# Kernel optimization log

Measured on AMD Instinct MI355X. Metric: run time of the kernel, lower is better.

Reference implementation:

```python
import jax, jax.numpy as jnp
import numpy as np

N_NODES = 100000
N_EDGES = 1600000
IN_CH = 128
DIM = 128
OUT_CH = 10
NUM_GRAPHS = 128
BN_EPS = 1e-5


def _bn_train(h, gamma, beta):
    # BatchNorm1d in training mode: batch statistics over the node axis
    mean = jnp.mean(h, axis=0)
    var = jnp.var(h, axis=0)
    return (h - mean) * jax.lax.rsqrt(var + BN_EPS) * gamma + beta


def _gin_conv(x, src, dst, W1, b1, gamma, beta, W2, b2):
    # GINConv with eps=0: nn(x + sum_{j in N(i)} x_j)
    agg = jax.ops.segment_sum(x[src], dst, num_segments=x.shape[0])  # [N, d]
    h = (x + agg) @ W1 + b1
    h = jax.nn.relu(_bn_train(h, gamma, beta))
    h = jax.nn.relu(h @ W2 + b2)
    return h


def setup_inputs() -> dict:
    key = jax.random.key(0)
    ks = jax.random.split(key, 16)
    s = 0.02
    inp = {
        "x": jax.random.normal(ks[0], (N_NODES, IN_CH), dtype=jnp.float32),
        "edge_index": jax.random.randint(ks[1], (2, N_EDGES), 0, N_NODES, dtype=jnp.int64),
        "batch": jnp.sort(jax.random.randint(ks[2], (N_NODES,), 0, NUM_GRAPHS, dtype=jnp.int64)),
        # conv1 MLP
        "W1a": jax.random.normal(ks[3], (IN_CH, DIM), dtype=jnp.float32) * s,
        "b1a": jnp.zeros((DIM,), jnp.float32),
        "ga": jnp.ones((DIM,), jnp.float32),
        "ba": jnp.zeros((DIM,), jnp.float32),
        "W2a": jax.random.normal(ks[4], (DIM, DIM), dtype=jnp.float32) * s,
        "b2a": jnp.zeros((DIM,), jnp.float32),
        # conv2 MLP
        "W1b": jax.random.normal(ks[5], (DIM, DIM), dtype=jnp.float32) * s,
        "b1b": jnp.zeros((DIM,), jnp.float32),
        "gb": jnp.ones((DIM,), jnp.float32),
        "bb": jnp.zeros((DIM,), jnp.float32),
        "W2b": jax.random.normal(ks[6], (DIM, DIM), dtype=jnp.float32) * s,
        "b2b": jnp.zeros((DIM,), jnp.float32),
        # readout linears
        "Wl1": jax.random.normal(ks[7], (DIM, DIM), dtype=jnp.float32) * s,
        "bl1": jnp.zeros((DIM,), jnp.float32),
        "Wl2": jax.random.normal(ks[8], (DIM, OUT_CH), dtype=jnp.float32) * s,
        "bl2": jnp.zeros((OUT_CH,), jnp.float32),
    }
    return inp


def reference(x, edge_index, batch, W1a, b1a, ga, ba, W2a, b2a,
              W1b, b1b, gb, bb, W2b, b2b, Wl1, bl1, Wl2, bl2):
    src, dst = edge_index[0], edge_index[1]
    h = _gin_conv(x, src, dst, W1a, b1a, ga, ba, W2a, b2a)
    h = _gin_conv(h, src, dst, W1b, b1b, gb, bb, W2b, b2b)
    pooled = jax.ops.segment_sum(h, batch, num_segments=NUM_GRAPHS)  # [G, d]
    out = jax.nn.relu(pooled @ Wl1 + bl1)
    # dropout p=0.5 is identity in deterministic/eval evaluation
    out = out @ Wl2 + bl2
    return out
```

## Files before the change

### kernel.cpp

```cpp
#include <hip/hip_runtime.h>

#define N_NODES    100000
#define N_EDGES    1600000
#define DIM        128
#define OUT_CH     10
#define NUM_GRAPHS 128
#define BN_EPS     1e-5f

#define BSHIFT   8
#define NB2      391
#define CAP2     5120

typedef __attribute__((ext_vector_type(8))) short short8;
typedef __attribute__((ext_vector_type(4))) float floatx4;

__device__ inline float bf2f(unsigned short u) {
    union { unsigned i; float f; } v; v.i = (unsigned)u << 16; return v.f;
}
__device__ inline unsigned short f2bf(float f) {
    union { float f; unsigned i; } v; v.f = f;
    unsigned r = (v.i + 0x7fffu + ((v.i >> 16) & 1u)) >> 16;
    return (unsigned short)r;
}

__device__ inline void async_cp16(const unsigned short* g, unsigned short* l) {
    __builtin_amdgcn_global_load_lds(
        (const __attribute__((address_space(1))) void*)g,
        (__attribute__((address_space(3))) void*)l, 16, 0, 0);
}

__global__ __launch_bounds__(256)
void k_bucket(const int* __restrict__ src, const int* __restrict__ dst,
              int* __restrict__ gcur, uint2* __restrict__ pairs) {
    __shared__ int h[NB2];
    int t = threadIdx.x;
    for (int i = t; i < NB2; i += 256) h[i] = 0;
    __syncthreads();
    int base = blockIdx.x * 4096;
    #pragma unroll
    for (int i = 0; i < 16; ++i) {
        int idx = base + i * 256 + t;
        if (idx < N_EDGES) atomicAdd(&h[dst[idx] >> BSHIFT], 1);
    }
    __syncthreads();
    for (int i = t; i < NB2; i += 256) h[i] = atomicAdd(&gcur[i], h[i]);
    __syncthreads();
    #pragma unroll
    for (int i = 0; i < 16; ++i) {
        int idx = base + i * 256 + t;
        if (idx < N_EDGES) {
            int d = dst[idx];
            int b = d >> BSHIFT;
            int pos = atomicAdd(&h[b], 1);
            if (pos < CAP2) pairs[(size_t)b * CAP2 + pos] = make_uint2((unsigned)src[idx], (unsigned)d);
        }
    }
}

__global__ void k_bscan(const int* __restrict__ gcur, int* __restrict__ bbase,
                        int* __restrict__ row_ptr) {
    __shared__ int sh[512];
    int t = threadIdx.x;
    int v = (t < NB2) ? min(gcur[t], CAP2) : 0;
    sh[t] = v; __syncthreads();
    for (int off = 1; off < 512; off <<= 1) {
        int tmp = (t >= off) ? sh[t - off] : 0;
        __syncthreads();
        sh[t] += tmp;
        __syncthreads();
    }
    if (t < NB2) bbase[t] = sh[t] - v;
    if (t == NB2 - 1) { bbase[NB2] = sh[t]; row_ptr[N_NODES] = sh[t]; }
}

__global__ __launch_bounds__(256)
void k_csr(const uint2* __restrict__ pairs, const int* __restrict__ gcur,
           const int* __restrict__ bbase, int* __restrict__ row_ptr,
           int* __restrict__ col) {
    __shared__ int hist[256];
    __shared__ int cur[256];
    int bi = blockIdx.x, t = threadIdx.x;
    hist[t] = 0; __syncthreads();
    int n = min(gcur[bi], CAP2);
    const uint2* P = pairs + (size_t)bi * CAP2;
    for (int i = t; i < n; i += 256)
        atomicAdd(&hist[P[i].y & 255], 1);
    __syncthreads();
    int self = hist[t];
    cur[t] = self; __syncthreads();
    for (int off = 1; off < 256; off <<= 1) {
        int tmp = (t >= off) ? cur[t - off] : 0;
        __syncthreads();
        cur[t] += tmp;
        __syncthreads();
    }
    int excl = cur[t] - self;
    int base = bbase[bi];
    int node = (bi << 8) + t;
    if (node < N_NODES) row_ptr[node] = base + excl;
    __syncthreads();
    cur[t] = base + excl;
    __syncthreads();
    for (int i = t; i < n; i += 256) {
        uint2 e = P[i];
        int pos = atomicAdd(&cur[e.y & 255], 1);
        col[pos] = (int)e.x;
    }
}

__global__ void k_cvt_x(const float* __restrict__ x, unsigned short* __restrict__ xb) {
    int idx = blockIdx.x * 256 + threadIdx.x;
    float4 v = ((const float4*)x)[idx];
    ushort4 o;
    o.x = f2bf(v.x); o.y = f2bf(v.y); o.z = f2bf(v.z); o.w = f2bf(v.w);
    ((ushort4*)xb)[idx] = o;
}

__global__ void k_prep_w(const float* __restrict__ W0, const float* __restrict__ W1,
                         const float* __restrict__ W2, const float* __restrict__ W3,
                         unsigned short* __restrict__ Wt) {
    const float* Ws[4] = {W0, W1, W2, W3};
    const float* W = Ws[blockIdx.y];
    unsigned short* o = Wt + blockIdx.y * (DIM * DIM);
    int idx = blockIdx.x * 256 + threadIdx.x;
    int n = idx >> 7, k = idx & 127;
    o[idx] = f2bf(W[k * DIM + n]);
}

__global__ void k_agg(const unsigned short* __restrict__ X,
                      unsigned short* __restrict__ Out,
                      const int* __restrict__ row_ptr, const int* __restrict__ col) {
    int wid = (blockIdx.x * 256 + threadIdx.x) >> 6;
    if (wid >= N_NODES) return;
    int lane = threadIdx.x & 63;
    int half = lane >> 5, m = lane & 31;
    const ushort4* X4 = (const ushort4*)X;

    float a0=0.f,a1=0.f,a2=0.f,a3=0.f;
    float c0=0.f,c1=0.f,c2=0.f,c3=0.f;
    if (half == 0) {
        ushort4 sv = X4[(size_t)wid * 32 + m];
        a0 = bf2f(sv.x); a1 = bf2f(sv.y); a2 = bf2f(sv.z); a3 = bf2f(sv.w);
    }
    int s = row_ptr[wid], e = row_ptr[wid + 1];
    int p = s + half;
    for (; p + 6 < e; p += 8) {
        int n0 = col[p], n1 = col[p + 2], n2 = col[p + 4], n3 = col[p + 6];
        ushort4 v0 = X4[(size_t)n0 * 32 + m];
        ushort4 v1 = X4[(size_t)n1 * 32 + m];
        ushort4 v2 = X4[(size_t)n2 * 32 + m];
        ushort4 v3 = X4[(size_t)n3 * 32 + m];
        a0 += bf2f(v0.x); a1 += bf2f(v0.y); a2 += bf2f(v0.z); a3 += bf2f(v0.w);
        c0 += bf2f(v1.x); c1 += bf2f(v1.y); c2 += bf2f(v1.z); c3 += bf2f(v1.w);
        a0 += bf2f(v2.x); a1 += bf2f(v2.y); a2 += bf2f(v2.z); a3 += bf2f(v2.w);
        c0 += bf2f(v3.x); c1 += bf2f(v3.y); c2 += bf2f(v3.z); c3 += bf2f(v3.w);
    }
    for (; p < e; p += 2) {
        ushort4 v = X4[(size_t)col[p] * 32 + m];
        a0 += bf2f(v.x); a1 += bf2f(v.y); a2 += bf2f(v.z); a3 += bf2f(v.w);
    }
    a0 += c0; a1 += c1; a2 += c2; a3 += c3;
    a0 += __shfl_xor(a0, 32);
    a1 += __shfl_xor(a1, 32);
    a2 += __shfl_xor(a2, 32);
    a3 += __shfl_xor(a3, 32);
    if (half == 0) {
        ushort4 o;
        o.x = f2bf(a0); o.y = f2bf(a1); o.z = f2bf(a2); o.w = f2bf(a3);
        ((ushort4*)Out)[(size_t)wid * 32 + m] = o;
    }
}

template<bool BN_LOAD, bool RELU_ST>
__global__ __launch_bounds__(256)
void k_gemm(const unsigned short* __restrict__ In, unsigned short* __restrict__ Out,
            const unsigned short* __restrict__ Wt, const float* __restrict__ bias,
            const float* __restrict__ scale, const float* __restrict__ shift) {
    __shared__ __align__(16) unsigned short sB[128 * 128];
    __shared__ float ssc[128], ssh[128];

    int t = threadIdx.x;
    int w = t >> 6, lane = t & 63;
    int r0 = blockIdx.x * 128;
    int m = lane & 15;
    int q = lane >> 4;

    int rowA0 = min(r0 + w * 32 + m,      N_NODES - 1);
    int rowA1 = min(r0 + w * 32 + 16 + m, N_NODES - 1);
    short8 a0[4], a1[4];
    #pragma unroll
    for (int kk = 0; kk < 4; ++kk) {
        a0[kk] = *(const short8*)(In + (size_t)rowA0 * 128 + kk * 32 + q * 8);
        a1[kk] = *(const short8*)(In + (size_t)rowA1 * 128 + kk * 32 + q * 8);
    }

    #pragma unroll
    for (int u = 0; u < 8; ++u) {
        int i = (w * 8 + u) * 64 + lane;
        int n = i >> 4, p = i & 15;
        async_cp16(Wt + n * 128 + ((p ^ (n & 7)) << 3), sB + (size_t)(w * 8 + u) * 512);
    }
    if (BN_LOAD && t < 128) { ssc[t] = scale[t]; ssh[t] = shift[t]; }
    __syncthreads();

    if (BN_LOAD) {
        #pragma unroll
        for (int kk = 0; kk < 4; ++kk) {
            int base = kk * 32 + q * 8;
            float4 c0 = *(const float4*)&ssc[base];
            float4 c1 = *(const float4*)&ssc[base + 4];
            float4 h0 = *(const float4*)&ssh[base];
            float4 h1 = *(const float4*)&ssh[base + 4];
            float sc[8] = {c0.x,c0.y,c0.z,c0.w,c1.x,c1.y,c1.z,c1.w};
            float sh[8] = {h0.x,h0.y,h0.z,h0.w,h1.x,h1.y,h1.z,h1.w};
            #pragma unroll
            for (int j = 0; j < 8; ++j) {
                float f0 = fmaxf(bf2f((unsigned short)a0[kk][j]) * sc[j] + sh[j], 0.f);
                float f1 = fmaxf(bf2f((unsigned short)a1[kk][j]) * sc[j] + sh[j], 0.f);
                a0[kk][j] = (short)f2bf(f0);
                a1[kk][j] = (short)f2bf(f1);
            }
        }
    }

    int sw = m & 7;
    floatx4 acc[2][8] = {};
    #pragma unroll
    for (int kk = 0; kk < 4; ++kk) {
        int cp = (kk * 4 + q) ^ sw;
        #pragma unroll
        for (int c = 0; c < 8; ++c) {
            int nr = c * 16 + m;
            short8 b = *(const short8*)&sB[nr * 128 + (cp << 3)];
            acc[0][c] = __builtin_amdgcn_mfma_f32_16x16x32_bf16(b, a0[kk], acc[0][c], 0, 0, 0);
            acc[1][c] = __builtin_amdgcn_mfma_f32_16x16x32_bf16(b, a1[kk], acc[1][c], 0, 0, 0);
        }
    }

    #pragma unroll
    for (int c = 0; c < 8; ++c) {
        int ch0 = c * 16 + q * 4;
        float4 bv = *(const float4*)(bias + ch0);
        #pragma unroll
        for (int h = 0; h < 2; ++h) {
            int node = r0 + w * 32 + h * 16 + m;
            if (node < N_NODES) {
                float v0 = acc[h][c][0] + bv.x;
                float v1 = acc[h][c][1] + bv.y;
                float v2 = acc[h][c][2] + bv.z;
                float v3 = acc[h][c][3] + bv.w;
                if (RELU_ST) {
                    v0 = fmaxf(v0, 0.f); v1 = fmaxf(v1, 0.f);
                    v2 = fmaxf(v2, 0.f); v3 = fmaxf(v3, 0.f);
                }
                ushort4 o;
                o.x = f2bf(v0); o.y = f2bf(v1); o.z = f2bf(v2); o.w = f2bf(v3);
                *(ushort4*)(Out + (size_t)node * 128 + ch0) = o;
            }
        }
    }
}

#define ST_BLOCKS 250
#define ST_ROWS   400
__global__ __launch_bounds__(256)
void k_stats(const unsigned short* __restrict__ H,
             float* __restrict__ ssum, float* __restrict__ ssq) {
    __shared__ float rs[8][128];
    __shared__ float rq[8][128];
    int t  = threadIdx.x;
    int cq = t & 31;
    int r  = t >> 5;
    int row0 = blockIdx.x * ST_ROWS;
    float s0=0,s1=0,s2=0,s3=0,q0=0,q1=0,q2=0,q3=0;
    for (int i = r; i < ST_ROWS; i += 8) {
        ushort4 v = *(const ushort4*)(H + (size_t)(row0 + i) * 128 + cq * 4);
        float f0=bf2f(v.x), f1=bf2f(v.y), f2=bf2f(v.z), f3=bf2f(v.w);
        s0+=f0; s1+=f1; s2+=f2; s3+=f3;
        q0+=f0*f0; q1+=f1*f1; q2+=f2*f2; q3+=f3*f3;
    }
    rs[r][cq*4+0]=s0; rs[r][cq*4+1]=s1; rs[r][cq*4+2]=s2; rs[r][cq*4+3]=s3;
    rq[r][cq*4+0]=q0; rq[r][cq*4+1]=q1; rq[r][cq*4+2]=q2; rq[r][cq*4+3]=q3;
    __syncthreads();
    if (t < 128) {
        float a = 0.f, b = 0.f;
        #pragma unroll
        for (int j = 0; j < 8; ++j) { a += rs[j][t]; b += rq[j][t]; }
        atomicAdd(&ssum[t], a);
        atomicAdd(&ssq [t], b);
    }
}

__global__ void k_bnfin(const float* __restrict__ sum, const float* __restrict__ sq,
                        const float* __restrict__ gamma, const float* __restrict__ beta,
                        float* __restrict__ scale, float* __restrict__ shift) {
    int c = threadIdx.x;
    if (c < DIM) {
        float m   = sum[c] * (1.0f / N_NODES);
        float var = sq[c] * (1.0f / N_NODES) - m * m;
        float inv = rsqrtf(var + BN_EPS);
        float sc  = gamma[c] * inv;
        scale[c] = sc;
        shift[c] = beta[c] - m * sc;
    }
}

#define POOL_BLOCKS 512
#define POOL_CHUNK  196
__global__ void k_pool(const unsigned short* __restrict__ h, const int* __restrict__ batch,
                       float* __restrict__ pooled) {
    int c  = threadIdx.x;
    int n0 = blockIdx.x * POOL_CHUNK;
    if (n0 >= N_NODES) return;
    int n1 = min(n0 + POOL_CHUNK, N_NODES);
    int g = batch[n0];
    float acc = 0.f;
    for (int i = n0; i < n1; ++i) {
        int gi = batch[i];
        if (gi != g) { atomicAdd(&pooled[g * DIM + c], acc); acc = 0.f; g = gi; }
        acc += bf2f(h[(size_t)i * DIM + c]);
    }
    atomicAdd(&pooled[g * DIM + c], acc);
}

__global__ void k_readout1(const float* __restrict__ pooled, const float* __restrict__ W,
                           const float* __restrict__ b, float* __restrict__ r1) {
    int idx = blockIdx.x * 256 + threadIdx.x;
    int g = idx >> 7, c = idx & 127;
    float s = b[c];
    const float* p = pooled + g * DIM;
    #pragma unroll 8
    for (int k = 0; k < DIM; ++k) s += p[k] * W[k * DIM + c];
    r1[idx] = fmaxf(s, 0.f);
}

__global__ void k_readout2(const float* __restrict__ r1, const float* __restrict__ W,
                           const float* __restrict__ b, float* __restrict__ out) {
    int idx = blockIdx.x * 256 + threadIdx.x;
    if (idx >= NUM_GRAPHS * OUT_CH) return;
    int g = idx / OUT_CH, c = idx % OUT_CH;
    float s = b[c];
    const float* r = r1 + g * DIM;
    #pragma unroll 8
    for (int k = 0; k < DIM; ++k) s += r[k] * W[k * OUT_CH + c];
    out[idx] = s;
}

extern "C" void kernel_launch(void* const* d_in, const int* in_sizes, int n_in,
                              void* d_out, int out_size, void* d_ws, size_t ws_size,
                              hipStream_t stream) {
    const float* x   = (const float*)d_in[0];
    const int*   ei  = (const int*)d_in[1];
    const int*   bat = (const int*)d_in[2];
    const float* W1a = (const float*)d_in[3];
    const float* b1a = (const float*)d_in[4];
    const float* ga  = (const float*)d_in[5];
    const float* ba  = (const float*)d_in[6];
    const float* W2a = (const float*)d_in[7];
    const float* b2a = (const float*)d_in[8];
    const float* W1b = (const float*)d_in[9];
    const float* b1b = (const float*)d_in[10];
    const float* gb  = (const float*)d_in[11];
    const float* bbt = (const float*)d_in[12];
    const float* W2b = (const float*)d_in[13];
    const float* b2b = (const float*)d_in[14];
    const float* Wl1 = (const float*)d_in[15];
    const float* bl1 = (const float*)d_in[16];
    const float* Wl2 = (const float*)d_in[17];
    const float* bl2 = (const float*)d_in[18];
    float* out = (float*)d_out;

    const int* src = ei;
    const int* dst = ei + N_EDGES;

    char* w = (char*)d_ws;
    size_t off = 0;
    auto alloc = [&](size_t bytes) -> char* {
        char* p = w + off; off += (bytes + 255) & ~(size_t)255; return p;
    };
    unsigned short* xb   = (unsigned short*)alloc((size_t)N_NODES * DIM * 2);
    unsigned short* nb0  = (unsigned short*)alloc((size_t)N_NODES * DIM * 2);
    unsigned short* nb1  = (unsigned short*)alloc((size_t)N_NODES * DIM * 2);
    unsigned short* Wtb  = (unsigned short*)alloc((size_t)4 * DIM * DIM * 2);
    uint2* pairs   = (uint2*)alloc((size_t)NB2 * CAP2 * 8);
    int*   row_ptr = (int*)  alloc((size_t)(N_NODES + 1) * 4);
    int*   col     = (int*)  alloc((size_t)N_EDGES * 4);
    int*   gcur    = (int*)  alloc((NB2 + 1) * 4);
    int*   bbase   = (int*)  alloc((NB2 + 1) * 4);
    float* ssumA   = (float*)alloc(DIM * 4);
    float* ssqA    = (float*)alloc(DIM * 4);
    float* ssumB   = (float*)alloc(DIM * 4);
    float* ssqB    = (float*)alloc(DIM * 4);
    float* scale   = (float*)alloc(DIM * 4);
    float* shift   = (float*)alloc(DIM * 4);
    float* pooled  = (float*)alloc((size_t)NUM_GRAPHS * DIM * 4);
    float* r1      = (float*)alloc((size_t)NUM_GRAPHS * DIM * 4);

    hipMemsetAsync(gcur,  0, (NB2 + 1) * 4, stream);
    hipMemsetAsync(ssumA, 0, DIM * 4 * 4, stream);
    hipMemsetAsync(pooled,0, (size_t)NUM_GRAPHS * DIM * 4, stream);

    k_bucket<<<(N_EDGES + 4095) / 4096, 256, 0, stream>>>(src, dst, gcur, pairs);
    k_bscan<<<1, 512, 0, stream>>>(gcur, bbase, row_ptr);
    k_csr<<<NB2, 256, 0, stream>>>(pairs, gcur, bbase, row_ptr, col);

    k_cvt_x<<<(N_NODES * DIM / 4) / 256, 256, 0, stream>>>(x, xb);
    k_prep_w<<<dim3(64, 4), 256, 0, stream>>>(W1a, W2a, W1b, W2b, Wtb);
    const unsigned short* Wt1a = Wtb;
    const unsigned short* Wt2a = Wtb + DIM * DIM;
    const unsigned short* Wt1b = Wtb + 2 * DIM * DIM;
    const unsigned short* Wt2b = Wtb + 3 * DIM * DIM;

    int agg_blocks  = (N_NODES * 64) / 256;
    int gemm_blocks = (N_NODES + 127) / 128;

    k_agg<<<agg_blocks, 256, 0, stream>>>(xb, nb0, row_ptr, col);
    k_gemm<false, false><<<gemm_blocks, 256, 0, stream>>>(nb0, nb1, Wt1a, b1a, nullptr, nullptr);
    k_stats<<<ST_BLOCKS, 256, 0, stream>>>(nb1, ssumA, ssqA);
    k_bnfin<<<1, 128, 0, stream>>>(ssumA, ssqA, ga, ba, scale, shift);
    k_gemm<true, true><<<gemm_blocks, 256, 0, stream>>>(nb1, nb0, Wt2a, b2a, scale, shift);
    k_agg<<<agg_blocks, 256, 0, stream>>>(nb0, nb1, row_ptr, col);
    k_gemm<false, false><<<gemm_blocks, 256, 0, stream>>>(nb1, nb0, Wt1b, b1b, nullptr, nullptr);
    k_stats<<<ST_BLOCKS, 256, 0, stream>>>(nb0, ssumB, ssqB);
    k_bnfin<<<1, 128, 0, stream>>>(ssumB, ssqB, gb, bbt, scale, shift);
    k_gemm<true, true><<<gemm_blocks, 256, 0, stream>>>(nb0, nb1, Wt2b, b2b, scale, shift);
    k_pool<<<POOL_BLOCKS, 128, 0, stream>>>(nb1, bat, pooled);
    k_readout1<<<(NUM_GRAPHS * DIM) / 256, 256, 0, stream>>>(pooled, Wl1, bl1, r1);
    k_readout2<<<(NUM_GRAPHS * OUT_CH + 255) / 256, 256, 0, stream>>>(r1, Wl2, bl2, out);
}
```

Measured before the change: 513.0 us.

## Fuse BN stats into GEMM epilogue, pack edge pairs, merge memsets and readouts

The BatchNorm sum and sum-of-squares are now accumulated in the first GEMM's epilogue through wave shuffles, LDS atomics and global atomics. The separate stats and finalize kernels are removed, and the scale and shift are computed inside the second GEMM. Edge bucket pairs are packed into 32 bits (src<<8 | low dst bits), which halves the pairs traffic. The memsets are folded into the convert kernel, and the two readout kernels are merged into one. Together these cut launches and one full read pass over the hidden activations. In exchange, stats now come from fp32 values before bf16 rounding, and more global float atomics run.

Result: no change. 514.2 us (+0.2%).

```diff
diff --git a/kernel.cpp b/kernel.cpp
--- a/kernel.cpp
+++ b/kernel.cpp
@@ -29,9 +29,36 @@
         (__attribute__((address_space(3))) void*)l, 16, 0, 0);
 }
 
+__global__ void k_cvt_x(const float* __restrict__ x, unsigned short* __restrict__ xb,
+                        int* __restrict__ gcur, float* __restrict__ stats4,
+                        float* __restrict__ pooled) {
+    int t = threadIdx.x;
+    if (blockIdx.x == 0) {
+        for (int i = t; i < NB2 + 1; i += 256) gcur[i] = 0;
+        for (int i = t; i < 4 * DIM; i += 256) stats4[i] = 0.f;
+        for (int i = t; i < NUM_GRAPHS * DIM; i += 256) pooled[i] = 0.f;
+    }
+    int idx = blockIdx.x * 256 + t;
+    float4 v = ((const float4*)x)[idx];
+    ushort4 o;
+    o.x = f2bf(v.x); o.y = f2bf(v.y); o.z = f2bf(v.z); o.w = f2bf(v.w);
+    ((ushort4*)xb)[idx] = o;
+}
+
+__global__ void k_prep_w(const float* __restrict__ W0, const float* __restrict__ W1,
+                         const float* __restrict__ W2, const float* __restrict__ W3,
+                         unsigned short* __restrict__ Wt) {
+    const float* Ws[4] = {W0, W1, W2, W3};
+    const float* W = Ws[blockIdx.y];
+    unsigned short* o = Wt + blockIdx.y * (DIM * DIM);
+    int idx = blockIdx.x * 256 + threadIdx.x;
+    int n = idx >> 7, k = idx & 127;
+    o[idx] = f2bf(W[k * DIM + n]);
+}
+
 __global__ __launch_bounds__(256)
 void k_bucket(const int* __restrict__ src, const int* __restrict__ dst,
-              int* __restrict__ gcur, uint2* __restrict__ pairs) {
+              int* __restrict__ gcur, unsigned* __restrict__ pairs) {
     __shared__ int h[NB2];
     int t = threadIdx.x;
     for (int i = t; i < NB2; i += 256) h[i] = 0;
@@ -52,7 +79,8 @@
             int d = dst[idx];
             int b = d >> BSHIFT;
             int pos = atomicAdd(&h[b], 1);
-            if (pos < CAP2) pairs[(size_t)b * CAP2 + pos] = make_uint2((unsigned)src[idx], (unsigned)d);
+            if (pos < CAP2)
+                pairs[(size_t)b * CAP2 + pos] = ((unsigned)src[idx] << 8) | (unsigned)(d & 255);
         }
     }
 }
@@ -74,7 +102,7 @@
 }
 
 __global__ __launch_bounds__(256)
-void k_csr(const uint2* __restrict__ pairs, const int* __restrict__ gcur,
+void k_csr(const unsigned* __restrict__ pairs, const int* __restrict__ gcur,
            const int* __restrict__ bbase, int* __restrict__ row_ptr,
            int* __restrict__ col) {
     __shared__ int hist[256];
@@ -82,9 +110,9 @@
     int bi = blockIdx.x, t = threadIdx.x;
     hist[t] = 0; __syncthreads();
     int n = min(gcur[bi], CAP2);
-    const uint2* P = pairs + (size_t)bi * CAP2;
+    const unsigned* P = pairs + (size_t)bi * CAP2;
     for (int i = t; i < n; i += 256)
-        atomicAdd(&hist[P[i].y & 255], 1);
+        atomicAdd(&hist[P[i] & 255u], 1);
     __syncthreads();
     int self = hist[t];
     cur[t] = self; __syncthreads();
@@ -102,29 +130,10 @@
     cur[t] = base + excl;
     __syncthreads();
     for (int i = t; i < n; i += 256) {
-        uint2 e = P[i];
-        int pos = atomicAdd(&cur[e.y & 255], 1);
-        col[pos] = (int)e.x;
-    }
-}
-
-__global__ void k_cvt_x(const float* __restrict__ x, unsigned short* __restrict__ xb) {
-    int idx = blockIdx.x * 256 + threadIdx.x;
-    float4 v = ((const float4*)x)[idx];
-    ushort4 o;
-    o.x = f2bf(v.x); o.y = f2bf(v.y); o.z = f2bf(v.z); o.w = f2bf(v.w);
-    ((ushort4*)xb)[idx] = o;
-}
-
-__global__ void k_prep_w(const float* __restrict__ W0, const float* __restrict__ W1,
-                         const float* __restrict__ W2, const float* __restrict__ W3,
-                         unsigned short* __restrict__ Wt) {
-    const float* Ws[4] = {W0, W1, W2, W3};
-    const float* W = Ws[blockIdx.y];
-    unsigned short* o = Wt + blockIdx.y * (DIM * DIM);
-    int idx = blockIdx.x * 256 + threadIdx.x;
-    int n = idx >> 7, k = idx & 127;
-    o[idx] = f2bf(W[k * DIM + n]);
+        unsigned e = P[i];
+        int pos = atomicAdd(&cur[e & 255u], 1);
+        col[pos] = (int)(e >> 8);
+    }
 }
 
 __global__ void k_agg(const unsigned short* __restrict__ X,
@@ -171,13 +180,16 @@
     }
 }
 
-template<bool BN_LOAD, bool RELU_ST>
+template<bool BN_LOAD, bool STATS, bool RELU_ST>
 __global__ __launch_bounds__(256)
 void k_gemm(const unsigned short* __restrict__ In, unsigned short* __restrict__ Out,
             const unsigned short* __restrict__ Wt, const float* __restrict__ bias,
-            const float* __restrict__ scale, const float* __restrict__ shift) {
+            const float* __restrict__ ssum_in, const float* __restrict__ ssq_in,
+            const float* __restrict__ gamma, const float* __restrict__ beta,
+            float* __restrict__ ssum_out, float* __restrict__ ssq_out) {
     __shared__ __align__(16) unsigned short sB[128 * 128];
     __shared__ float ssc[128], ssh[128];
+    __shared__ float s_sum[128], s_sq[128];
 
     int t = threadIdx.x;
     int w = t >> 6, lane = t & 63;
@@ -200,23 +212,25 @@
         int n = i >> 4, p = i & 15;
         async_cp16(Wt + n * 128 + ((p ^ (n & 7)) << 3), sB + (size_t)(w * 8 + u) * 512);
     }
-    if (BN_LOAD && t < 128) { ssc[t] = scale[t]; ssh[t] = shift[t]; }
+    if (BN_LOAD && t < 128) {
+        float mn  = ssum_in[t] * (1.0f / N_NODES);
+        float var = ssq_in[t] * (1.0f / N_NODES) - mn * mn;
+        float inv = rsqrtf(var + BN_EPS);
+        float sc  = gamma[t] * inv;
+        ssc[t] = sc; ssh[t] = beta[t] - mn * sc;
+    }
+    if (STATS && t < 128) { s_sum[t] = 0.f; s_sq[t] = 0.f; }
     __syncthreads();
 
     if (BN_LOAD) {
         #pragma unroll
         for (int kk = 0; kk < 4; ++kk) {
             int base = kk * 32 + q * 8;
-            float4 c0 = *(const float4*)&ssc[base];
-            float4 c1 = *(const float4*)&ssc[base + 4];
-            float4 h0 = *(const float4*)&ssh[base];
-            float4 h1 = *(const float4*)&ssh[base + 4];
-            float sc[8] = {c0.x,c0.y,c0.z,c0.w,c1.x,c1.y,c1.z,c1.w};
-            float sh[8] = {h0.x,h0.y,h0.z,h0.w,h1.x,h1.y,h1.z,h1.w};
             #pragma unroll
             for (int j = 0; j < 8; ++j) {
-                float f0 = fmaxf(bf2f((unsigned short)a0[kk][j]) * sc[j] + sh[j], 0.f);
-                float f1 = fmaxf(bf2f((unsigned short)a1[kk][j]) * sc[j] + sh[j], 0.f);
+                float scj = ssc[base + j], shj = ssh[base + j];
+                float f0 = fmaxf(bf2f((unsigned short)a0[kk][j]) * scj + shj, 0.f);
+                float f1 = fmaxf(bf2f((unsigned short)a1[kk][j]) * scj + shj, 0.f);
                 a0[kk][j] = (short)f2bf(f0);
                 a1[kk][j] = (short)f2bf(f1);
             }
@@ -241,67 +255,52 @@
     for (int c = 0; c < 8; ++c) {
         int ch0 = c * 16 + q * 4;
         float4 bv = *(const float4*)(bias + ch0);
+        float sr[4] = {0,0,0,0}, qr[4] = {0,0,0,0};
         #pragma unroll
         for (int h = 0; h < 2; ++h) {
             int node = r0 + w * 32 + h * 16 + m;
+            float v0 = acc[h][c][0] + bv.x;
+            float v1 = acc[h][c][1] + bv.y;
+            float v2 = acc[h][c][2] + bv.z;
+            float v3 = acc[h][c][3] + bv.w;
+            if (RELU_ST) {
+                v0 = fmaxf(v0, 0.f); v1 = fmaxf(v1, 0.f);
+                v2 = fmaxf(v2, 0.f); v3 = fmaxf(v3, 0.f);
+            }
             if (node < N_NODES) {
-                float v0 = acc[h][c][0] + bv.x;
-                float v1 = acc[h][c][1] + bv.y;
-                float v2 = acc[h][c][2] + bv.z;
-                float v3 = acc[h][c][3] + bv.w;
-                if (RELU_ST) {
-                    v0 = fmaxf(v0, 0.f); v1 = fmaxf(v1, 0.f);
-                    v2 = fmaxf(v2, 0.f); v3 = fmaxf(v3, 0.f);
-                }
                 ushort4 o;
                 o.x = f2bf(v0); o.y = f2bf(v1); o.z = f2bf(v2); o.w = f2bf(v3);
                 *(ushort4*)(Out + (size_t)node * 128 + ch0) = o;
+                if (STATS) {
+                    sr[0] += v0; sr[1] += v1; sr[2] += v2; sr[3] += v3;
+                    qr[0] += v0*v0; qr[1] += v1*v1; qr[2] += v2*v2; qr[3] += v3*v3;
+                }
             }
         }
-    }
-}
-
-#define ST_BLOCKS 250
-#define ST_ROWS   400
-__global__ __launch_bounds__(256)
-void k_stats(const unsigned short* __restrict__ H,
-             float* __restrict__ ssum, float* __restrict__ ssq) {
-    __shared__ float rs[8][128];
-    __shared__ float rq[8][128];
-    int t  = threadIdx.x;
-    int cq = t & 31;
-    int r  = t >> 5;
-    int row0 = blockIdx.x * ST_ROWS;
-    float s0=0,s1=0,s2=0,s3=0,q0=0,q1=0,q2=0,q3=0;
-    for (int i = r; i < ST_ROWS; i += 8) {
-        ushort4 v = *(const ushort4*)(H + (size_t)(row0 + i) * 128 + cq * 4);
-        float f0=bf2f(v.x), f1=bf2f(v.y), f2=bf2f(v.z), f3=bf2f(v.w);
-        s0+=f0; s1+=f1; s2+=f2; s3+=f3;
-        q0+=f0*f0; q1+=f1*f1; q2+=f2*f2; q3+=f3*f3;
-    }
-    rs[r][cq*4+0]=s0; rs[r][cq*4+1]=s1; rs[r][cq*4+2]=s2; rs[r][cq*4+3]=s3;
-    rq[r][cq*4+0]=q0; rq[r][cq*4+1]=q1; rq[r][cq*4+2]=q2; rq[r][cq*4+3]=q3;
-    __syncthreads();
-    if (t < 128) {
-        float a = 0.f, b = 0.f;
-        #pragma unroll
-        for (int j = 0; j < 8; ++j) { a += rs[j][t]; b += rq[j][t]; }
-        atomicAdd(&ssum[t], a);
-        atomicAdd(&ssq [t], b);
-    }
-}
-
-__global__ void k_bnfin(const float* __restrict__ sum, const float* __restrict__ sq,
-                        const float* __restrict__ gamma, const float* __restrict__ beta,
-                        float* __restrict__ scale, float* __restrict__ shift) {
-    int c = threadIdx.x;
-    if (c < DIM) {
-        float m   = sum[c] * (1.0f / N_NODES);
-        float var = sq[c] * (1.0f / N_NODES) - m * m;
-        float inv = rsqrtf(var + BN_EPS);
-        float sc  = gamma[c] * inv;
-        scale[c] = sc;
-        shift[c] = beta[c] - m * sc;
+        if (STATS) {
+            #pragma unroll
+            for (int msk = 1; msk <= 8; msk <<= 1) {
+                #pragma unroll
+                for (int r = 0; r < 4; ++r) {
+                    sr[r] += __shfl_xor(sr[r], msk);
+                    qr[r] += __shfl_xor(qr[r], msk);
+                }
+            }
+            if (m == 0) {
+                #pragma unroll
+                for (int r = 0; r < 4; ++r) {
+                    atomicAdd(&s_sum[ch0 + r], sr[r]);
+                    atomicAdd(&s_sq [ch0 + r], qr[r]);
+                }
+            }
+        }
+    }
+    if (STATS) {
+        __syncthreads();
+        if (t < 128) {
+            atomicAdd(&ssum_out[t], s_sum[t]);
+            atomicAdd(&ssq_out [t], s_sq[t]);
+        }
     }
 }
 
@@ -323,27 +322,25 @@
     atomicAdd(&pooled[g * DIM + c], acc);
 }
 
-__global__ void k_readout1(const float* __restrict__ pooled, const float* __restrict__ W,
-                           const float* __restrict__ b, float* __restrict__ r1) {
-    int idx = blockIdx.x * 256 + threadIdx.x;
-    int g = idx >> 7, c = idx & 127;
-    float s = b[c];
-    const float* p = pooled + g * DIM;
+__global__ void k_readout(const float* __restrict__ pooled,
+                          const float* __restrict__ Wl1, const float* __restrict__ bl1,
+                          const float* __restrict__ Wl2, const float* __restrict__ bl2,
+                          float* __restrict__ out) {
+    __shared__ float p[128], r[128];
+    int g = blockIdx.x, c = threadIdx.x;
+    p[c] = pooled[g * DIM + c];
+    __syncthreads();
+    float s = bl1[c];
     #pragma unroll 8
-    for (int k = 0; k < DIM; ++k) s += p[k] * W[k * DIM + c];
-    r1[idx] = fmaxf(s, 0.f);
-}
-
-__global__ void k_readout2(const float* __restrict__ r1, const float* __restrict__ W,
-                           const float* __restrict__ b, float* __restrict__ out) {
-    int idx = blockIdx.x * 256 + threadIdx.x;
-    if (idx >= NUM_GRAPHS * OUT_CH) return;
-    int g = idx / OUT_CH, c = idx % OUT_CH;
-    float s = b[c];
-    const float* r = r1 + g * DIM;
-    #pragma unroll 8
-    for (int k = 0; k < DIM; ++k) s += r[k] * W[k * OUT_CH + c];
-    out[idx] = s;
+    for (int k = 0; k < DIM; ++k) s += p[k] * Wl1[k * DIM + c];
+    r[c] = fmaxf(s, 0.f);
+    __syncthreads();
+    if (c < OUT_CH) {
+        float s2 = bl2[c];
+        #pragma unroll 8
+        for (int k = 0; k < DIM; ++k) s2 += r[k] * Wl2[k * OUT_CH + c];
+        out[g * OUT_CH + c] = s2;
+    }
 }
 
 extern "C" void kernel_launch(void* const* d_in, const int* in_sizes, int n_in,
@@ -382,49 +379,39 @@
     unsigned short* nb0  = (unsigned short*)alloc((size_t)N_NODES * DIM * 2);
     unsigned short* nb1  = (unsigned short*)alloc((size_t)N_NODES * DIM * 2);
     unsigned short* Wtb  = (unsigned short*)alloc((size_t)4 * DIM * DIM * 2);
-    uint2* pairs   = (uint2*)alloc((size_t)NB2 * CAP2 * 8);
+    unsigned* pairs = (unsigned*)alloc((size_t)NB2 * CAP2 * 4);
     int*   row_ptr = (int*)  alloc((size_t)(N_NODES + 1) * 4);
     int*   col     = (int*)  alloc((size_t)N_EDGES * 4);
     int*   gcur    = (int*)  alloc((NB2 + 1) * 4);
     int*   bbase   = (int*)  alloc((NB2 + 1) * 4);
-    float* ssumA   = (float*)alloc(DIM * 4);
-    float* ssqA    = (float*)alloc(DIM * 4);
-    float* ssumB   = (float*)alloc(DIM * 4);
-    float* ssqB    = (float*)alloc(DIM * 4);
-    float* scale   = (float*)alloc(DIM * 4);
-    float* shift   = (float*)alloc(DIM * 4);
+    float* stats4  = (float*)alloc((size_t)4 * DIM * 4);
     float* pooled  = (float*)alloc((size_t)NUM_GRAPHS * DIM * 4);
-    float* r1      = (float*)alloc((size_t)NUM_GRAPHS * DIM * 4);
-
-    hipMemsetAsync(gcur,  0, (NB2 + 1) * 4, stream);
-    hipMemsetAsync(ssumA, 0, DIM * 4 * 4, stream);
-    hipMemsetAsync(pooled,0, (size_t)NUM_GRAPHS * DIM * 4, stream);
-
-    k_bucket<<<(N_EDGES + 4095) / 4096, 256, 0, stream>>>(src, dst, gcur, pairs);
-    k_bscan<<<1, 512, 0, stream>>>(gcur, bbase, row_ptr);
-    k_csr<<<NB2, 256, 0, stream>>>(pairs, gcur, bbase, row_ptr, col);
-
-    k_cvt_x<<<(N_NODES * DIM / 4) / 256, 256, 0, stream>>>(x, xb);
+    float* ssumA = stats4, *ssqA = stats4 + DIM, *ssumB = stats4 + 2*DIM, *ssqB = stats4 + 3*DIM;
+
+    k_cvt_x<<<(N_NODES * DIM / 4) / 256, 256, 0, stream>>>(x, xb, gcur, stats4, pooled);
     k_prep_w<<<dim3(64, 4), 256, 0, stream>>>(W1a, W2a, W1b, W2b, Wtb);
     const unsigned short* Wt1a = Wtb;
     const unsigned short* Wt2a = Wtb + DIM * DIM;
     const unsigned short* Wt1b = Wtb + 2 * DIM * DIM;
     const unsigned short* Wt2b = Wtb + 3 * DIM * DIM;
 
+    k_bucket<<<(N_EDGES + 4095) / 4096, 256, 0, stream>>>(src, dst, gcur, pairs);
+    k_bscan<<<1, 512, 0, stream>>>(gcur, bbase, row_ptr);
+    k_csr<<<NB2, 256, 0, stream>>>(pairs, gcur, bbase, row_ptr, col);
+
     int agg_blocks  = (N_NODES * 64) / 256;
     int gemm_blocks = (N_NODES + 127) / 128;
 
     k_agg<<<agg_blocks, 256, 0, stream>>>(xb, nb0, row_ptr, col);
-    k_gemm<false, false><<<gemm_blocks, 256, 0, stream>>>(nb0, nb1, Wt1a, b1a, nullptr, nullptr);
-    k_stats<<<ST_BLOCKS, 256, 0, stream>>>(nb1, ssumA, ssqA);
-    k_bnfin<<<1, 128, 0, stream>>>(ssumA, ssqA, ga, ba, scale, shift);
-    k_gemm<true, true><<<gemm_blocks, 256, 0, stream>>>(nb1, nb0, Wt2a, b2a, scale, shift);
+    k_gemm<false, true, false><<<gemm_blocks, 256, 0, stream>>>(
+        nb0, nb1, Wt1a, b1a, nullptr, nullptr, nullptr, nullptr, ssumA, ssqA);
+    k_gemm<true, false, true><<<gemm_blocks, 256, 0, stream>>>(
+        nb1, nb0, Wt2a, b2a, ssumA, ssqA, ga, ba, nullptr, nullptr);
     k_agg<<<agg_blocks, 256, 0, stream>>>(nb0, nb1, row_ptr, col);
-    k_gemm<false, false><<<gemm_blocks, 256, 0, stream>>>(nb1, nb0, Wt1b, b1b, nullptr, nullptr);
-    k_stats<<<ST_BLOCKS, 256, 0, stream>>>(nb0, ssumB, ssqB);
-    k_bnfin<<<1, 128, 0, stream>>>(ssumB, ssqB, gb, bbt, scale, shift);
-    k_gemm<true, true><<<gemm_blocks, 256, 0, stream>>>(nb0, nb1, Wt2b, b2b, scale, shift);
+    k_gemm<false, true, false><<<gemm_blocks, 256, 0, stream>>>(
+        nb1, nb0, Wt1b, b1b, nullptr, nullptr, nullptr, nullptr, ssumB, ssqB);
+    k_gemm<true, false, true><<<gemm_blocks, 256, 0, stream>>>(
+        nb0, nb1, Wt2b, b2b, ssumB, ssqB, gb, bbt, nullptr, nullptr);
     k_pool<<<POOL_BLOCKS, 128, 0, stream>>>(nb1, bat, pooled);
-    k_readout1<<<(NUM_GRAPHS * DIM) / 256, 256, 0, stream>>>(pooled, Wl1, bl1, r1);
-    k_readout2<<<(NUM_GRAPHS * OUT_CH + 255) / 256, 256, 0, stream>>>(r1, Wl2, bl2, out);
-}
+    k_readout<<<NUM_GRAPHS, 128, 0, stream>>>(pooled, Wl1, bl1, Wl2, bl2, out);
+}
```
